# Kernel optimization log

Hardware: AMD Instinct MI355X
Metric: run time of the kernel (lower is better)

The kernel has to match this reference:

```python
import jax, jax.numpy as jnp
import numpy as np

N, E, F_IN, D, L = 100000, 1600000, 32, 128, 5
B, V, T, EMB = 3000, 64, 128, 64
H = L * D  # 640 LSTM hidden
BN_EPS = 1e-5


def setup_inputs():
    key = jax.random.key(0)
    ks = jax.random.split(key, 20)
    rn = lambda k, s, sc=0.05: jax.random.normal(k, s, jnp.float32) * sc
    inp = {
        'x': jax.random.normal(ks[0], (N, F_IN), jnp.float32),
        'edge_index': jax.random.randint(ks[1], (2, E), 0, N, jnp.int32),
        'batch': jnp.sort(jax.random.randint(ks[2], (N,), 0, B, jnp.int32)),
        'smi': jax.random.randint(ks[3], (B, T), 0, V, jnp.int32),
        'gin0_w1': rn(ks[4], (F_IN, D)), 'gin0_b1': jnp.zeros((D,), jnp.float32),
        'gin0_w2': rn(ks[5], (D, D)),    'gin0_b2': jnp.zeros((D,), jnp.float32),
        'ginr_w1': rn(ks[6], (L - 1, D, D)), 'ginr_b1': jnp.zeros((L - 1, D), jnp.float32),
        'ginr_w2': rn(ks[7], (L - 1, D, D)), 'ginr_b2': jnp.zeros((L - 1, D), jnp.float32),
        'bn_gamma': jnp.ones((L, D), jnp.float32), 'bn_beta': jnp.zeros((L, D), jnp.float32),
        'emb': rn(ks[8], (V, EMB), 0.1).at[0].set(0.0),  # padding_idx=0
        'w_ih': rn(ks[9], (4 * H, EMB), 0.04), 'w_hh': rn(ks[10], (4 * H, H), 0.04),
        'b_ih': jnp.zeros((4 * H,), jnp.float32), 'b_hh': jnp.zeros((4 * H,), jnp.float32),
        'g_w1': rn(ks[11], (L * D, 4 * D)), 'g_b1': jnp.zeros((4 * D,), jnp.float32),
        'g_bn_gamma': jnp.ones((4 * D,), jnp.float32), 'g_bn_beta': jnp.zeros((4 * D,), jnp.float32),
        'g_w2': rn(ks[12], (4 * D, 6 * D)),
    }
    return inp


def _bn(h, gamma, beta):
    # BatchNorm1d in training mode: biased batch statistics
    mu = h.mean(0)
    var = h.var(0)
    return (h - mu) * jax.lax.rsqrt(var + BN_EPS) * gamma + beta


def _gin_layer(h, src, dst, w1, b1, w2, b2, gamma, beta):
    # GINConv (eps=0): MLP(x + sum_{j->i} x_j), then ReLU, then BN
    agg = jax.ops.segment_sum(h[src], dst, num_segments=N)  # [N, d]
    z = h + agg
    z = jnp.maximum(z @ w1 + b1, 0.0) @ w2 + b2
    z = jnp.maximum(z, 0.0)
    return _bn(z, gamma, beta)


def _lstm_last(e, w_ih, w_hh, b_ih, b_hh):
    # e: [B, T, EMB] -> last hidden state [B, H]
    def step(carry, xt):
        h, c = carry
        gates = xt @ w_ih.T + b_ih + h @ w_hh.T + b_hh  # [B, 4H]
        i, f, g, o = jnp.split(gates, 4, axis=1)  # torch gate order i,f,g,o
        c = jax.nn.sigmoid(f) * c + jax.nn.sigmoid(i) * jnp.tanh(g)
        h = jax.nn.sigmoid(o) * jnp.tanh(c)
        return (h, c), None
    h0 = jnp.zeros((e.shape[0], H), e.dtype)
    (h, _), _ = jax.lax.scan(step, (h0, h0), e.transpose(1, 0, 2))
    return h


def reference(x, edge_index, batch, smi, gin0_w1, gin0_b1, gin0_w2, gin0_b2,
              ginr_w1, ginr_b1, ginr_w2, ginr_b2, bn_gamma, bn_beta, emb,
              w_ih, w_hh, b_ih, b_hh, g_w1, g_b1, g_bn_gamma, g_bn_beta, g_w2):
    src, dst = edge_index[0], edge_index[1]
    # --- GIN encoder with layer-wise global_add_pool ---
    h = _gin_layer(x, src, dst, gin0_w1, gin0_b1, gin0_w2, gin0_b2, bn_gamma[0], bn_beta[0])
    pools = [jax.ops.segment_sum(h, batch, num_segments=B)]
    for i in range(L - 1):
        h = _gin_layer(h, src, dst, ginr_w1[i], ginr_b1[i], ginr_w2[i], ginr_b2[i],
                       bn_gamma[i + 1], bn_beta[i + 1])
        pools.append(jax.ops.segment_sum(h, batch, num_segments=B))
    enc1 = jnp.concatenate(pools, axis=1)  # [B, L*D]
    # --- SMILES encoder: Embedding + LSTM, take output at last timestep ---
    enc2 = _lstm_last(emb[smi], w_ih, w_hh, b_ih, b_hh)  # [B, H] == [B, L*D]
    # --- shared projection head g, L2-normalized (F.normalize, eps=1e-12) ---
    def g_head(z):
        z1 = jnp.maximum(_bn(z @ g_w1 + g_b1, g_bn_gamma, g_bn_beta), 0.0)
        out = z1 @ g_w2
        nrm = jnp.maximum(jnp.linalg.norm(out, axis=1, keepdims=True), 1e-12)
        return out / nrm
    return (g_head(enc1), g_head(enc2))
```

## Files before the change

kernel.cpp:

```cpp
#include <hip/hip_runtime.h>

typedef __bf16 bf16x8 __attribute__((ext_vector_type(8)));
typedef float f32x4 __attribute__((ext_vector_type(4)));
typedef unsigned short ushort8 __attribute__((ext_vector_type(8)));

#define DEV static __device__ __forceinline__

DEV unsigned short f2bf(float f){
  unsigned int u = __builtin_bit_cast(unsigned int, f);
  u += 0x7fffu + ((u >> 16) & 1u);
  return (unsigned short)(u >> 16);
}
DEV float bf2f(unsigned short u){
  return __builtin_bit_cast(float, ((unsigned int)u) << 16);
}
DEV float sigf(float x){ return 1.0f/(1.0f + __expf(-x)); }

static constexpr int NN   = 100000;
static constexpr int NPAD = 100096;
static constexpr int NE   = 1600000;
static constexpr int NB   = 3000;
static constexpr int BPAD = 3072;
static constexpr int TT   = 128;
static constexpr int HID  = 640;
static constexpr int SCAN_B = 1024;
static constexpr int NBLK = (NN + SCAN_B - 1)/SCAN_B;

__global__ void cvt_k(const float* __restrict__ s, unsigned short* __restrict__ d, int n){
  int i = blockIdx.x*256 + threadIdx.x; if (i < n) d[i] = f2bf(s[i]);
}
__global__ void transpose_cvt_split_k(const float* __restrict__ s, unsigned short* __restrict__ dh,
                                      unsigned short* __restrict__ dl, int R, int C){
  int i = blockIdx.x*256 + threadIdx.x; if (i >= R*C) return;
  int r = i / C, c = i - r*C;
  float v = s[i];
  unsigned short hi = f2bf(v);
  dh[c*R + r] = hi;
  dl[c*R + r] = f2bf(v - bf2f(hi));
}
__global__ void wc_build_k(const float* __restrict__ whh, const float* __restrict__ wih,
                           unsigned short* __restrict__ wc){
  int i = blockIdx.x*256 + threadIdx.x; if (i >= 2560*704) return;
  int n = i / 704, k = i - n*704;
  float v = (k < 640) ? whh[n*640 + k] : wih[n*64 + (k - 640)];
  wc[i] = f2bf(v);
}
__global__ void add_k(const float* __restrict__ a, const float* __restrict__ b, float* __restrict__ o, int n){
  int i = blockIdx.x*256 + threadIdx.x; if (i < n) o[i] = a[i] + b[i];
}

__global__ __launch_bounds__(256) void deg_hist_k(const int* __restrict__ dsts, int* __restrict__ deg){
  int e = blockIdx.x*256 + threadIdx.x; if (e < NE) atomicAdd(&deg[dsts[e]], 1);
}
__global__ __launch_bounds__(256) void scan_bsum_k(const int* __restrict__ deg, int* __restrict__ bsum){
  __shared__ int red[4];
  int b = blockIdx.x, tid = threadIdx.x;
  int base = b*SCAN_B + tid*4;
  int s = 0;
  #pragma unroll
  for (int q = 0; q < 4; ++q){ int idx = base + q; s += (idx < NN) ? deg[idx] : 0; }
  #pragma unroll
  for (int m = 1; m < 64; m <<= 1) s += __shfl_xor(s, m);
  if ((tid & 63) == 0) red[tid >> 6] = s;
  __syncthreads();
  if (tid == 0) bsum[b] = red[0] + red[1] + red[2] + red[3];
}
__global__ void scan_off_k(int* __restrict__ bsum){
  if (threadIdx.x == 0){
    int run = 0;
    for (int i = 0; i < NBLK; ++i){ int t = bsum[i]; bsum[i] = run; run += t; }
  }
}
__global__ __launch_bounds__(256) void scan_write_k(const int* __restrict__ deg, const int* __restrict__ bsum,
                                                    int* __restrict__ rowptr, int* __restrict__ cursor){
  __shared__ int tsum[256];
  int b = blockIdx.x, tid = threadIdx.x;
  int base = b*SCAN_B + tid*4;
  int v[4]; int s = 0;
  #pragma unroll
  for (int q = 0; q < 4; ++q){ int idx = base + q; v[q] = (idx < NN) ? deg[idx] : 0; s += v[q]; }
  tsum[tid] = s;
  __syncthreads();
  for (int offt = 1; offt < 256; offt <<= 1){
    int y = (tid >= offt) ? tsum[tid - offt] : 0;
    __syncthreads();
    tsum[tid] += y;
    __syncthreads();
  }
  int run = bsum[b] + tsum[tid] - s;
  #pragma unroll
  for (int q = 0; q < 4; ++q){
    int idx = base + q;
    if (idx < NN){ rowptr[idx] = run; cursor[idx] = run; }
    run += v[q];
  }
  if (b == 0 && tid == 0) rowptr[NN] = NE;
}
__global__ __launch_bounds__(256) void csr_fill_k(const int* __restrict__ srcs, const int* __restrict__ dsts,
                                                  int* __restrict__ cursor, int* __restrict__ eidx){
  int e = blockIdx.x*256 + threadIdx.x; if (e >= NE) return;
  int d = dsts[e];
  int pos = atomicAdd(&cursor[d], 1);
  eidx[pos] = srcs[e];
}

__global__ __launch_bounds__(256) void gbound_k(const int* __restrict__ batch, int* __restrict__ gstart){
  int i = blockIdx.x*256 + threadIdx.x;
  if (i >= NN) return;
  int bi = batch[i];
  int bp = (i == 0) ? -1 : batch[i-1];
  for (int g = bp + 1; g <= bi; ++g) gstart[g] = i;
  if (i == NN-1){
    for (int g = bi + 1; g <= NB; ++g) gstart[g] = NN;
  }
}

__global__ __launch_bounds__(256) void agg128_k(const int* __restrict__ rowptr, const int* __restrict__ eidx,
    const float* __restrict__ H, float* __restrict__ Z){
  int wid = (blockIdx.x*256 + threadIdx.x) >> 6;
  if (wid >= NN) return;
  int lane = threadIdx.x & 63;
  const float2* Hp = (const float2*)H;
  int n0 = rowptr[wid], n1 = rowptr[wid+1];
  float2 acc = Hp[(size_t)wid*64 + lane];
  int i = n0;
  for (; i + 1 < n1; i += 2){
    int s0 = eidx[i], s1 = eidx[i+1];
    float2 v0 = Hp[(size_t)s0*64 + lane];
    float2 v1 = Hp[(size_t)s1*64 + lane];
    acc.x += v0.x + v1.x; acc.y += v0.y + v1.y;
  }
  if (i < n1){
    float2 v = Hp[(size_t)eidx[i]*64 + lane];
    acc.x += v.x; acc.y += v.y;
  }
  ((float2*)Z)[(size_t)wid*64 + lane] = acc;
}
__global__ __launch_bounds__(256) void agg32_k(const int* __restrict__ rowptr, const int* __restrict__ eidx,
    const float* __restrict__ X, float* __restrict__ Z){
  int r = (blockIdx.x*256 + threadIdx.x) >> 5;
  if (r >= NN) return;
  int l = threadIdx.x & 31;
  int n0 = rowptr[r], n1 = rowptr[r+1];
  float acc = X[(size_t)r*32 + l];
  int i = n0;
  for (; i + 1 < n1; i += 2){
    int s0 = eidx[i], s1 = eidx[i+1];
    acc += X[(size_t)s0*32 + l] + X[(size_t)s1*32 + l];
  }
  if (i < n1) acc += X[(size_t)eidx[i]*32 + l];
  Z[(size_t)r*32 + l] = acc;
}

template<int KIN>
__global__ __launch_bounds__(256) void gin_mlp_k(const float* __restrict__ Z,
    const unsigned short* __restrict__ W1h, const unsigned short* __restrict__ W1l,
    const unsigned short* __restrict__ W2h, const unsigned short* __restrict__ W2l,
    const float* __restrict__ b1, const float* __restrict__ b2,
    float* __restrict__ Y, float* __restrict__ stats)
{
  constexpr int SA = KIN + 8;
  __shared__ __align__(16) unsigned short Ah[128*136];
  __shared__ __align__(16) unsigned short Al[128*136];
  const int tid = threadIdx.x, lane = tid & 63, w = tid >> 6;
  const int row0 = blockIdx.x * 128;
  const int wr = (w >> 1)*64, wc0 = (w & 1)*64;
  const int l15 = lane & 15, lg = lane >> 4;

  constexpr int CH = KIN/8;
  #pragma unroll
  for (int i = 0; i < (128*CH)/256; ++i){
    int chunk = tid + 256*i;
    int row = chunk / CH, kc = (chunk - row*CH)*8;
    const float* sp = Z + (size_t)(row0 + row)*KIN + kc;
    float4 a0 = *(const float4*)sp;
    float4 a1 = *(const float4*)(sp + 4);
    float vv[8] = {a0.x,a0.y,a0.z,a0.w,a1.x,a1.y,a1.z,a1.w};
    ushort8 vh, vl;
    #pragma unroll
    for (int q=0;q<8;++q){ unsigned short h = f2bf(vv[q]); vh[q]=h; vl[q]=f2bf(vv[q]-bf2f(h)); }
    *(ushort8*)&Ah[row*SA + kc] = vh;
    *(ushort8*)&Al[row*SA + kc] = vl;
  }
  __syncthreads();

  f32x4 acc[4][4];
  #pragma unroll
  for (int i=0;i<4;++i)
    #pragma unroll
    for (int j=0;j<4;++j) acc[i][j] = (f32x4)(0.0f);

  #pragma unroll
  for (int k0 = 0; k0 < KIN; k0 += 32){
    bf16x8 ah[4], al[4], bh[4], bl[4];
    #pragma unroll
    for (int fa=0; fa<4; ++fa){
      ah[fa] = *(const bf16x8*)&Ah[(wr + fa*16 + l15)*SA + k0 + 8*lg];
      al[fa] = *(const bf16x8*)&Al[(wr + fa*16 + l15)*SA + k0 + 8*lg];
    }
    #pragma unroll
    for (int fb=0; fb<4; ++fb){
      bh[fb] = *(const bf16x8*)&W1h[(wc0 + fb*16 + l15)*KIN + k0 + 8*lg];
      bl[fb] = *(const bf16x8*)&W1l[(wc0 + fb*16 + l15)*KIN + k0 + 8*lg];
    }
    #pragma unroll
    for (int fa=0; fa<4; ++fa)
      #pragma unroll
      for (int fb=0; fb<4; ++fb){
        acc[fa][fb] = __builtin_amdgcn_mfma_f32_16x16x32_bf16(ah[fa], bh[fb], acc[fa][fb], 0, 0, 0);
        acc[fa][fb] = __builtin_amdgcn_mfma_f32_16x16x32_bf16(al[fa], bh[fb], acc[fa][fb], 0, 0, 0);
        acc[fa][fb] = __builtin_amdgcn_mfma_f32_16x16x32_bf16(ah[fa], bl[fb], acc[fa][fb], 0, 0, 0);
      }
  }
  __syncthreads();

  {
    float b1v[4];
    #pragma unroll
    for (int fb=0; fb<4; ++fb) b1v[fb] = b1[wc0 + fb*16 + l15];
    #pragma unroll
    for (int fa=0; fa<4; ++fa)
      #pragma unroll
      for (int fb=0; fb<4; ++fb)
        #pragma unroll
        for (int r=0; r<4; ++r){
          float v = fmaxf(acc[fa][fb][r] + b1v[fb], 0.0f);
          unsigned short h = f2bf(v);
          int idx = (wr + fa*16 + lg*4 + r)*136 + (wc0 + fb*16 + l15);
          Ah[idx] = h;
          Al[idx] = f2bf(v - bf2f(h));
        }
  }
  __syncthreads();

  f32x4 acc2[4][4];
  #pragma unroll
  for (int i=0;i<4;++i)
    #pragma unroll
    for (int j=0;j<4;++j) acc2[i][j] = (f32x4)(0.0f);

  #pragma unroll
  for (int k0 = 0; k0 < 128; k0 += 32){
    bf16x8 ah[4], al[4], bh[4], bl[4];
    #pragma unroll
    for (int fa=0; fa<4; ++fa){
      ah[fa] = *(const bf16x8*)&Ah[(wr + fa*16 + l15)*136 + k0 + 8*lg];
      al[fa] = *(const bf16x8*)&Al[(wr + fa*16 + l15)*136 + k0 + 8*lg];
    }
    #pragma unroll
    for (int fb=0; fb<4; ++fb){
      bh[fb] = *(const bf16x8*)&W2h[(wc0 + fb*16 + l15)*128 + k0 + 8*lg];
      bl[fb] = *(const bf16x8*)&W2l[(wc0 + fb*16 + l15)*128 + k0 + 8*lg];
    }
    #pragma unroll
    for (int fa=0; fa<4; ++fa)
      #pragma unroll
      for (int fb=0; fb<4; ++fb){
        acc2[fa][fb] = __builtin_amdgcn_mfma_f32_16x16x32_bf16(ah[fa], bh[fb], acc2[fa][fb], 0, 0, 0);
        acc2[fa][fb] = __builtin_amdgcn_mfma_f32_16x16x32_bf16(al[fa], bh[fb], acc2[fa][fb], 0, 0, 0);
        acc2[fa][fb] = __builtin_amdgcn_mfma_f32_16x16x32_bf16(ah[fa], bl[fb], acc2[fa][fb], 0, 0, 0);
      }
  }

  float b2v[4]; int cc[4];
  #pragma unroll
  for (int fb=0; fb<4; ++fb){ cc[fb] = wc0 + fb*16 + l15; b2v[fb] = b2[cc[fb]]; }
  float ps[4] = {0,0,0,0}, pq[4] = {0,0,0,0};
  #pragma unroll
  for (int fa=0; fa<4; ++fa)
    #pragma unroll
    for (int fb=0; fb<4; ++fb)
      #pragma unroll
      for (int r=0; r<4; ++r){
        int row = row0 + wr + fa*16 + lg*4 + r;
        float v = fmaxf(acc2[fa][fb][r] + b2v[fb], 0.0f);
        if (row < NN){
          Y[(size_t)row*128 + cc[fb]] = v;
          ps[fb] += v; pq[fb] += v*v;
        }
      }
  #pragma unroll
  for (int fb=0; fb<4; ++fb){
    float s = ps[fb]; s += __shfl_xor(s, 16); s += __shfl_xor(s, 32);
    float q = pq[fb]; q += __shfl_xor(q, 16); q += __shfl_xor(q, 32);
    if (lane < 16){ atomicAdd(&stats[cc[fb]], s); atomicAdd(&stats[128 + cc[fb]], q); }
  }
}

__global__ void bn_finalize_k(const float* __restrict__ stats, const float* __restrict__ gamma,
                              const float* __restrict__ beta, float* __restrict__ sshift, int C, float invN){
  int c = blockIdx.x*blockDim.x + threadIdx.x; if (c >= C) return;
  float mean = stats[c]*invN;
  float var  = fmaxf(stats[C+c]*invN - mean*mean, 0.0f);
  float inv  = rsqrtf(var + 1e-5f);
  float sc   = gamma[c]*inv;
  sshift[c] = sc; sshift[C+c] = beta[c] - mean*sc;
}

__global__ __launch_bounds__(256) void bn_apply_k(const float* __restrict__ Y,
    const float* __restrict__ sshift, float* __restrict__ Hb)
{
  int gid = blockIdx.x*256 + threadIdx.x;
  int r = gid >> 5;
  if (r >= NN) return;
  int c0 = (gid & 31) << 2;
  float4 y = *(const float4*)&Y[(size_t)r*128 + c0];
  float4 h;
  h.x = y.x*sshift[c0+0] + sshift[128+c0+0];
  h.y = y.y*sshift[c0+1] + sshift[128+c0+1];
  h.z = y.z*sshift[c0+2] + sshift[128+c0+2];
  h.w = y.w*sshift[c0+3] + sshift[128+c0+3];
  *(float4*)&Hb[(size_t)r*128 + c0] = h;
}

__global__ __launch_bounds__(256) void pool_seg_k(const float* __restrict__ Hb,
    const int* __restrict__ gstart, float* __restrict__ pool, int layer)
{
  int g = blockIdx.x*4 + (threadIdx.x >> 6);
  if (g >= NB) return;
  int lane = threadIdx.x & 63;
  int n0 = gstart[g], n1 = gstart[g+1];
  const float2* Hp = (const float2*)Hb;
  float2 acc = make_float2(0.f, 0.f);
  for (int r = n0; r < n1; ++r){
    float2 v = Hp[(size_t)r*64 + lane];
    acc.x += v.x; acc.y += v.y;
  }
  ((float2*)pool)[(size_t)g*320 + layer*64 + lane] = acc;
}

__global__ __launch_bounds__(256) void embed_k(const int* __restrict__ smi,
    const unsigned short* __restrict__ emb_bf, unsigned short* __restrict__ e_bf){
  int gid = blockIdx.x*256 + threadIdx.x;
  int b = gid >> 11;
  if (b >= BPAD) return;
  int t = (gid >> 4) & 127;
  int k4 = (gid & 15) << 2;
  uint2 v = make_uint2(0u, 0u);
  if (b < NB){
    int tok = smi[b*TT + t];
    v = *(const uint2*)&emb_bf[tok*64 + k4];
  }
  *(uint2*)&e_bf[(size_t)(b*TT + t)*64 + k4] = v;
}

__global__ __launch_bounds__(256) void lstm_step_k(const unsigned short* __restrict__ hprev,
    unsigned short* __restrict__ hnext, float* __restrict__ cbuf,
    const unsigned short* __restrict__ ebf, const unsigned short* __restrict__ Wc,
    const float* __restrict__ biasc, int t, float* __restrict__ hfin)
{
  __shared__ __align__(16) unsigned short As[128*40];
  __shared__ __align__(16) unsigned short Bs[128*40];
  const int tid = threadIdx.x, lane = tid & 63, w = tid >> 6;
  const int row0 = blockIdx.x * 128;
  const int j0 = blockIdx.y * 32;
  const int l15 = lane & 15, lg = lane >> 4;

  f32x4 acc[2][8];
  #pragma unroll
  for (int i=0;i<2;++i)
    #pragma unroll
    for (int j=0;j<8;++j) acc[i][j] = (f32x4)(0.0f);

  for (int kk = 0; kk < 22; ++kk){
    const int k0 = kk*32;
    #pragma unroll
    for (int i = 0; i < 2; ++i){
      int chunk = tid + 256*i;
      int row = chunk >> 2, kc = (chunk & 3) << 3;
      ushort8 v;
      if (k0 < 640) v = *(const ushort8*)&hprev[(size_t)(row0+row)*HID + k0 + kc];
      else          v = *(const ushort8*)&ebf[(size_t)((row0+row)*TT + t)*64 + (k0-640) + kc];
      *(ushort8*)&As[row*40 + kc] = v;
      int c = row;
      int ng = (c >> 5)*640 + j0 + (c & 31);
      *(ushort8*)&Bs[c*40 + kc] = *(const ushort8*)&Wc[(size_t)ng*704 + k0 + kc];
    }
    __syncthreads();
    bf16x8 a[2], b[8];
    #pragma unroll
    for (int fa=0; fa<2; ++fa) a[fa] = *(const bf16x8*)&As[(w*32 + fa*16 + l15)*40 + 8*lg];
    #pragma unroll
    for (int fb=0; fb<8; ++fb) b[fb] = *(const bf16x8*)&Bs[(fb*16 + l15)*40 + 8*lg];
    #pragma unroll
    for (int fa=0; fa<2; ++fa)
      #pragma unroll
      for (int fb=0; fb<8; ++fb)
        acc[fa][fb] = __builtin_amdgcn_mfma_f32_16x16x32_bf16(a[fa], b[fb], acc[fa][fb], 0, 0, 0);
    __syncthreads();
  }

  #pragma unroll
  for (int fa=0; fa<2; ++fa){
    #pragma unroll
    for (int par=0; par<2; ++par){
      int jj = j0 + par*16 + l15;
      float bi = biasc[jj], bf_ = biasc[640+jj], bg = biasc[1280+jj], bo = biasc[1920+jj];
      #pragma unroll
      for (int r=0; r<4; ++r){
        int br = row0 + w*32 + fa*16 + lg*4 + r;
        float iv = acc[fa][0+par][r] + bi;
        float fv = acc[fa][2+par][r] + bf_;
        float gv = acc[fa][4+par][r] + bg;
        float ov = acc[fa][6+par][r] + bo;
        size_t idx = (size_t)br*HID + jj;
        float co = cbuf[idx];
        float cn = sigf(fv)*co + sigf(iv)*tanhf(gv);
        cbuf[idx] = cn;
        float hv = sigf(ov)*tanhf(cn);
        hnext[idx] = f2bf(hv);
        if (hfin) hfin[idx] = hv;
      }
    }
  }
}

template<int DO_STATS>
__global__ __launch_bounds__(256) void gemm_split_k(const float* __restrict__ A,
    const unsigned short* __restrict__ Bh, const unsigned short* __restrict__ Bl,
    const float* __restrict__ bias, float* __restrict__ outp, float* __restrict__ stats,
    int Mvalid, int Nc, int K)
{
  __shared__ __align__(16) unsigned short Ah[128*40];
  __shared__ __align__(16) unsigned short Al[128*40];
  const int tid = threadIdx.x, lane = tid & 63, w = tid >> 6;
  const int row0 = blockIdx.x * 128, col0 = blockIdx.y * 128;
  const int wr = (w >> 1)*64, wc0 = (w & 1)*64;
  const int l15 = lane & 15, lg = lane >> 4;

  f32x4 acc[4][4];
  #pragma unroll
  for (int i=0;i<4;++i)
    #pragma unroll
    for (int j=0;j<4;++j) acc[i][j] = (f32x4)(0.0f);

  for (int k0 = 0; k0 < K; k0 += 32){
    #pragma unroll
    for (int i=0;i<2;++i){
      int chunk = tid + 256*i;
      int row = chunk >> 2, kc = (chunk & 3) << 3;
      const float* sp = A + (size_t)(row0+row)*K + k0 + kc;
      float4 a0 = *(const float4*)sp;
      float4 a1 = *(const float4*)(sp + 4);
      float vv[8] = {a0.x,a0.y,a0.z,a0.w,a1.x,a1.y,a1.z,a1.w};
      ushort8 vh, vl;
      #pragma unroll
      for (int q=0;q<8;++q){ unsigned short h = f2bf(vv[q]); vh[q]=h; vl[q]=f2bf(vv[q]-bf2f(h)); }
      *(ushort8*)&Ah[row*40 + kc] = vh;
      *(ushort8*)&Al[row*40 + kc] = vl;
    }
    __syncthreads();
    bf16x8 ah[4], al[4], bh[4], bl[4];
    #pragma unroll
    for (int fa=0; fa<4; ++fa){
      ah[fa] = *(const bf16x8*)&Ah[(wr + fa*16 + l15)*40 + 8*lg];
      al[fa] = *(const bf16x8*)&Al[(wr + fa*16 + l15)*40 + 8*lg];
    }
    #pragma unroll
    for (int fb=0; fb<4; ++fb){
      bh[fb] = *(const bf16x8*)&Bh[(size_t)(col0 + wc0 + fb*16 + l15)*K + k0 + 8*lg];
      bl[fb] = *(const bf16x8*)&Bl[(size_t)(col0 + wc0 + fb*16 + l15)*K + k0 + 8*lg];
    }
    #pragma unroll
    for (int fa=0; fa<4; ++fa)
      #pragma unroll
      for (int fb=0; fb<4; ++fb){
        acc[fa][fb] = __builtin_amdgcn_mfma_f32_16x16x32_bf16(ah[fa], bh[fb], acc[fa][fb], 0, 0, 0);
        acc[fa][fb] = __builtin_amdgcn_mfma_f32_16x16x32_bf16(al[fa], bh[fb], acc[fa][fb], 0, 0, 0);
        acc[fa][fb] = __builtin_amdgcn_mfma_f32_16x16x32_bf16(ah[fa], bl[fb], acc[fa][fb], 0, 0, 0);
      }
    __syncthreads();
  }

  float bv[4]; int cc[4];
  #pragma unroll
  for (int fb=0; fb<4; ++fb){ cc[fb] = col0 + wc0 + fb*16 + l15; bv[fb] = bias ? bias[cc[fb]] : 0.0f; }
  float ps[4] = {0,0,0,0}, pq[4] = {0,0,0,0};
  #pragma unroll
  for (int fa=0; fa<4; ++fa)
    #pragma unroll
    for (int fb=0; fb<4; ++fb)
      #pragma unroll
      for (int r=0; r<4; ++r){
        int row = row0 + wr + fa*16 + lg*4 + r;
        float v = acc[fa][fb][r] + bv[fb];
        if (row < Mvalid){
          outp[(size_t)row*Nc + cc[fb]] = v;
          if (DO_STATS){ ps[fb] += v; pq[fb] += v*v; }
        }
      }
  if (DO_STATS){
    #pragma unroll
    for (int fb=0; fb<4; ++fb){
      float s = ps[fb]; s += __shfl_xor(s, 16); s += __shfl_xor(s, 32);
      float q = pq[fb]; q += __shfl_xor(q, 16); q += __shfl_xor(q, 32);
      if (lane < 16){ atomicAdd(&stats[cc[fb]], s); atomicAdd(&stats[Nc + cc[fb]], q); }
    }
  }
}

__global__ __launch_bounds__(256) void bn_apply_head_k(const float* __restrict__ Zpre,
    const float* __restrict__ sshift, float* __restrict__ z1f){
  int gid = blockIdx.x*256 + threadIdx.x;
  int r = gid >> 7;
  if (r >= BPAD) return;
  int c0 = (gid & 127) << 2;
  float4 o = make_float4(0.f,0.f,0.f,0.f);
  if (r < NB){
    float4 v = *(const float4*)&Zpre[(size_t)r*512 + c0];
    o.x = fmaxf(v.x*sshift[c0+0] + sshift[512+c0+0], 0.0f);
    o.y = fmaxf(v.y*sshift[c0+1] + sshift[512+c0+1], 0.0f);
    o.z = fmaxf(v.z*sshift[c0+2] + sshift[512+c0+2], 0.0f);
    o.w = fmaxf(v.w*sshift[c0+3] + sshift[512+c0+3], 0.0f);
  }
  *(float4*)&z1f[(size_t)r*512 + c0] = o;
}

__global__ __launch_bounds__(256) void rownorm_k(const float* __restrict__ in, float* __restrict__ outp){
  int r = blockIdx.x;
  const float* p = in + (size_t)r*768;
  float ss = 0.0f;
  #pragma unroll
  for (int i = 0; i < 3; ++i){ float v = p[threadIdx.x + 256*i]; ss += v*v; }
  #pragma unroll
  for (int m = 1; m < 64; m <<= 1) ss += __shfl_xor(ss, m);
  __shared__ float red[4];
  if ((threadIdx.x & 63) == 0) red[threadIdx.x >> 6] = ss;
  __syncthreads();
  float tot = red[0] + red[1] + red[2] + red[3];
  float inv = 1.0f / fmaxf(sqrtf(tot), 1e-12f);
  float* q = outp + (size_t)r*768;
  #pragma unroll
  for (int i = 0; i < 3; ++i) q[threadIdx.x + 256*i] = p[threadIdx.x + 256*i]*inv;
}

static inline int cdiv(long a, long b){ return (int)((a + b - 1)/b); }

extern "C" void kernel_launch(void* const* d_in, const int* in_sizes, int n_in,
                              void* d_out, int out_size, void* d_ws, size_t ws_size,
                              hipStream_t stream)
{
  const float* x        = (const float*)d_in[0];
  const int*   edges    = (const int*)d_in[1];
  const int*   batch    = (const int*)d_in[2];
  const int*   smi      = (const int*)d_in[3];
  const float* gin0_w1  = (const float*)d_in[4];
  const float* gin0_b1  = (const float*)d_in[5];
  const float* gin0_w2  = (const float*)d_in[6];
  const float* gin0_b2  = (const float*)d_in[7];
  const float* ginr_w1  = (const float*)d_in[8];
  const float* ginr_b1  = (const float*)d_in[9];
  const float* ginr_w2  = (const float*)d_in[10];
  const float* ginr_b2  = (const float*)d_in[11];
  const float* bn_gamma = (const float*)d_in[12];
  const float* bn_beta  = (const float*)d_in[13];
  const float* emb      = (const float*)d_in[14];
  const float* w_ih     = (const float*)d_in[15];
  const float* w_hh     = (const float*)d_in[16];
  const float* b_ih     = (const float*)d_in[17];
  const float* b_hh     = (const float*)d_in[18];
  const float* g_w1     = (const float*)d_in[19];
  const float* g_b1     = (const float*)d_in[20];
  const float* g_bng    = (const float*)d_in[21];
  const float* g_bnb    = (const float*)d_in[22];
  const float* g_w2     = (const float*)d_in[23];
  float* outp = (float*)d_out;
  const int* srcs = edges;
  const int* dsts = edges + NE;

  char* base = (char*)d_ws;
  size_t off = 0;
  auto carve = [&](size_t bytes)->char*{ char* p = base + off; off += (bytes + 255) & ~(size_t)255; return p; };
  float* z_gin = (float*)carve((size_t)NPAD*128*4);
  float* y_gin = (float*)carve((size_t)NPAD*128*4);
  float* h_gin = (float*)carve((size_t)NPAD*128*4);
  float* pool  = (float*)carve((size_t)BPAD*HID*4);
  unsigned short* Wc     = (unsigned short*)carve((size_t)2560*704*2);
  float*          biasc  = (float*)carve(2560*4);
  unsigned short* emb_bf = (unsigned short*)carve(4096*2);
  unsigned short* w1t0h  = (unsigned short*)carve(128*32*2);
  unsigned short* w1t0l  = (unsigned short*)carve(128*32*2);
  unsigned short* w2t0h  = (unsigned short*)carve(128*128*2);
  unsigned short* w2t0l  = (unsigned short*)carve(128*128*2);
  unsigned short* w1trh  = (unsigned short*)carve(4*16384*2);
  unsigned short* w1trl  = (unsigned short*)carve(4*16384*2);
  unsigned short* w2trh  = (unsigned short*)carve(4*16384*2);
  unsigned short* w2trl  = (unsigned short*)carve(4*16384*2);
  unsigned short* gw1th  = (unsigned short*)carve(512*640*2);
  unsigned short* gw1tl  = (unsigned short*)carve(512*640*2);
  unsigned short* gw2th  = (unsigned short*)carve(768*512*2);
  unsigned short* gw2tl  = (unsigned short*)carve(768*512*2);
  float* stats  = (float*)carve(1024*4);
  float* sshift = (float*)carve(1024*4);
  int* deg    = (int*)carve((size_t)NN*4);
  int* cursor = (int*)carve((size_t)NN*4);
  int* rowptr = (int*)carve((size_t)(NN+1)*4);
  int* bsum   = (int*)carve(512);
  int* eidx   = (int*)carve((size_t)NE*4);
  int* gstart = (int*)carve((size_t)(NB+1)*4);

  unsigned short* e_bf   = (unsigned short*)y_gin;
  unsigned short* h_a    = (unsigned short*)h_gin;
  unsigned short* h_b    = h_a + (size_t)BPAD*HID;
  float*          c_buf  = (float*)(h_b + (size_t)BPAD*HID);
  float*          hfin   = c_buf + (size_t)BPAD*HID;
  float*          z1pre  = (float*)z_gin;
  float*          z1f    = z1pre + (size_t)BPAD*512;
  float*          outtmp = z1f + (size_t)BPAD*512;

  wc_build_k<<<cdiv((long)2560*704,256),256,0,stream>>>(w_hh, w_ih, Wc);
  add_k<<<cdiv(2560,256),256,0,stream>>>(b_ih, b_hh, biasc, 2560);
  cvt_k<<<cdiv(4096,256),256,0,stream>>>(emb, emb_bf, 4096);
  transpose_cvt_split_k<<<cdiv(32*128,256),256,0,stream>>>(gin0_w1, w1t0h, w1t0l, 32, 128);
  transpose_cvt_split_k<<<cdiv(16384,256),256,0,stream>>>(gin0_w2, w2t0h, w2t0l, 128, 128);
  for (int i = 0; i < 4; ++i){
    transpose_cvt_split_k<<<cdiv(16384,256),256,0,stream>>>(ginr_w1 + (size_t)i*16384, w1trh + (size_t)i*16384, w1trl + (size_t)i*16384, 128, 128);
    transpose_cvt_split_k<<<cdiv(16384,256),256,0,stream>>>(ginr_w2 + (size_t)i*16384, w2trh + (size_t)i*16384, w2trl + (size_t)i*16384, 128, 128);
  }
  transpose_cvt_split_k<<<cdiv(640*512,256),256,0,stream>>>(g_w1, gw1th, gw1tl, 640, 512);
  transpose_cvt_split_k<<<cdiv(512*768,256),256,0,stream>>>(g_w2, gw2th, gw2tl, 512, 768);

  hipMemsetAsync(deg, 0, (size_t)NN*4, stream);
  deg_hist_k<<<cdiv(NE,256),256,0,stream>>>(dsts, deg);
  scan_bsum_k<<<NBLK,256,0,stream>>>(deg, bsum);
  scan_off_k<<<1,64,0,stream>>>(bsum);
  scan_write_k<<<NBLK,256,0,stream>>>(deg, bsum, rowptr, cursor);
  csr_fill_k<<<cdiv(NE,256),256,0,stream>>>(srcs, dsts, cursor, eidx);
  gbound_k<<<cdiv(NN,256),256,0,stream>>>(batch, gstart);

  for (int l = 0; l < 5; ++l){
    hipMemsetAsync(stats, 0, 1024*4, stream);
    if (l == 0)
      agg32_k<<<cdiv((long)NN*32,256),256,0,stream>>>(rowptr, eidx, x, z_gin);
    else
      agg128_k<<<cdiv((long)NN*64,256),256,0,stream>>>(rowptr, eidx, h_gin, z_gin);
    if (l == 0)
      gin_mlp_k<32><<<NPAD/128,256,0,stream>>>(z_gin, w1t0h, w1t0l, w2t0h, w2t0l, gin0_b1, gin0_b2, y_gin, stats);
    else
      gin_mlp_k<128><<<NPAD/128,256,0,stream>>>(z_gin, w1trh + (size_t)(l-1)*16384, w1trl + (size_t)(l-1)*16384,
                                                w2trh + (size_t)(l-1)*16384, w2trl + (size_t)(l-1)*16384,
                                                ginr_b1 + (l-1)*128, ginr_b2 + (l-1)*128, y_gin, stats);
    bn_finalize_k<<<1,128,0,stream>>>(stats, bn_gamma + l*128, bn_beta + l*128, sshift, 128, 1.0f/NN);
    bn_apply_k<<<cdiv((long)NN*32,256),256,0,stream>>>(y_gin, sshift, h_gin);
    pool_seg_k<<<cdiv(NB,4),256,0,stream>>>(h_gin, gstart, pool, l);
  }

  embed_k<<<cdiv((long)BPAD*TT*16,256),256,0,stream>>>(smi, emb_bf, e_bf);
  hipMemsetAsync(h_a, 0, (size_t)BPAD*HID*2, stream);
  hipMemsetAsync(c_buf, 0, (size_t)BPAD*HID*4, stream);
  for (int t = 0; t < TT; ++t){
    const unsigned short* hin = (t & 1) ? h_b : h_a;
    unsigned short* hout      = (t & 1) ? h_a : h_b;
    lstm_step_k<<<dim3(BPAD/128, 20),256,0,stream>>>(hin, hout, c_buf, e_bf, Wc, biasc, t,
                                                     (t == TT-1) ? hfin : nullptr);
  }

  const float* headAf[2] = { pool, hfin };
  for (int hd = 0; hd < 2; ++hd){
    hipMemsetAsync(stats, 0, 1024*4, stream);
    gemm_split_k<1><<<dim3(BPAD/128, 4),256,0,stream>>>(headAf[hd], gw1th, gw1tl, g_b1, z1pre, stats, NB, 512, 640);
    bn_finalize_k<<<2,256,0,stream>>>(stats, g_bng, g_bnb, sshift, 512, 1.0f/NB);
    bn_apply_head_k<<<cdiv((long)BPAD*128,256),256,0,stream>>>(z1pre, sshift, z1f);
    gemm_split_k<0><<<dim3(BPAD/128, 6),256,0,stream>>>(z1f, gw2th, gw2tl, nullptr, outtmp, nullptr, NB, 768, 512);
    rownorm_k<<<NB,256,0,stream>>>(outtmp, outp + (size_t)hd*NB*768);
  }
}
```

Baseline: 4.965 ms.

## Double-buffer LSTM step GEMM and pre-permute gate weights into contiguous tiles

The LSTM step kernel now uses double-buffered LDS tiles, issuing global loads for the next K-slice into registers while MFMAs run on the current slice. It also moves from a 2x8 to a 2x2 wave layout with 4x4 fragments per wave. To support this, the combined W_hh/W_ih weight matrix is permuted once so each block's 128 gate rows are contiguous. The embedding buffer is reordered to time-major so each step reads a contiguous slab. The cost is twice the LDS use, which may lower occupancy, and more index math in the one-time weight build.

```diff
diff --git a/kernel.cpp b/kernel.cpp
--- a/kernel.cpp
+++ b/kernel.cpp
@@ -38,12 +38,15 @@
   dh[c*R + r] = hi;
   dl[c*R + r] = f2bf(v - bf2f(hi));
 }
-__global__ void wc_build_k(const float* __restrict__ whh, const float* __restrict__ wih,
-                           unsigned short* __restrict__ wc){
+__global__ void wc2_build_k(const float* __restrict__ whh, const float* __restrict__ wih,
+                            unsigned short* __restrict__ wc2){
   int i = blockIdx.x*256 + threadIdx.x; if (i >= 2560*704) return;
-  int n = i / 704, k = i - n*704;
+  int n2 = i / 704, k = i - n2*704;
+  int jt = n2 >> 7, rem = n2 & 127;
+  int hc = rem >> 6, gate = (rem >> 4) & 3, j15 = rem & 15;
+  int n = gate*640 + jt*32 + hc*16 + j15;
   float v = (k < 640) ? whh[n*640 + k] : wih[n*64 + (k - 640)];
-  wc[i] = f2bf(v);
+  wc2[i] = f2bf(v);
 }
 __global__ void add_k(const float* __restrict__ a, const float* __restrict__ b, float* __restrict__ o, int n){
   int i = blockIdx.x*256 + threadIdx.x; if (i < n) o[i] = a[i] + b[i];
@@ -330,87 +333,106 @@
 }
 
 __global__ __launch_bounds__(256) void embed_k(const int* __restrict__ smi,
-    const unsigned short* __restrict__ emb_bf, unsigned short* __restrict__ e_bf){
+    const unsigned short* __restrict__ emb_bf, unsigned short* __restrict__ e2){
   int gid = blockIdx.x*256 + threadIdx.x;
-  int b = gid >> 11;
-  if (b >= BPAD) return;
-  int t = (gid >> 4) & 127;
+  int tb = gid >> 4;
+  if (tb >= TT*BPAD) return;
+  int t = tb / BPAD, b = tb - t*BPAD;
   int k4 = (gid & 15) << 2;
   uint2 v = make_uint2(0u, 0u);
   if (b < NB){
     int tok = smi[b*TT + t];
     v = *(const uint2*)&emb_bf[tok*64 + k4];
   }
-  *(uint2*)&e_bf[(size_t)(b*TT + t)*64 + k4] = v;
+  *(uint2*)&e2[(size_t)tb*64 + k4] = v;
 }
 
 __global__ __launch_bounds__(256) void lstm_step_k(const unsigned short* __restrict__ hprev,
     unsigned short* __restrict__ hnext, float* __restrict__ cbuf,
-    const unsigned short* __restrict__ ebf, const unsigned short* __restrict__ Wc,
+    const unsigned short* __restrict__ e2, const unsigned short* __restrict__ Wc2,
     const float* __restrict__ biasc, int t, float* __restrict__ hfin)
 {
-  __shared__ __align__(16) unsigned short As[128*40];
-  __shared__ __align__(16) unsigned short Bs[128*40];
+  __shared__ __align__(16) unsigned short As[2][128*40];
+  __shared__ __align__(16) unsigned short Bs[2][128*40];
   const int tid = threadIdx.x, lane = tid & 63, w = tid >> 6;
   const int row0 = blockIdx.x * 128;
-  const int j0 = blockIdx.y * 32;
+  const int jt = blockIdx.y;
   const int l15 = lane & 15, lg = lane >> 4;
-
-  f32x4 acc[2][8];
-  #pragma unroll
-  for (int i=0;i<2;++i)
-    #pragma unroll
-    for (int j=0;j<8;++j) acc[i][j] = (f32x4)(0.0f);
-
+  const int wr = (w >> 1)*64, wc0 = (w & 1)*64;
+
+  const int srow = tid >> 2, skc = (tid & 3) << 3;
+  const unsigned short* A0 = hprev + (size_t)(row0 + srow)*HID;
+  const unsigned short* A1 = hprev + (size_t)(row0 + srow + 64)*HID;
+  const unsigned short* E0 = e2 + ((size_t)t*BPAD + row0 + srow)*64;
+  const unsigned short* E1 = e2 + ((size_t)t*BPAD + row0 + srow + 64)*64;
+  const unsigned short* B0 = Wc2 + (size_t)(jt*128 + srow)*704;
+  const unsigned short* B1 = Wc2 + (size_t)(jt*128 + srow + 64)*704;
+
+  *(ushort8*)&As[0][srow*40 + skc]      = *(const ushort8*)&A0[skc];
+  *(ushort8*)&As[0][(srow+64)*40 + skc] = *(const ushort8*)&A1[skc];
+  *(ushort8*)&Bs[0][srow*40 + skc]      = *(const ushort8*)&B0[skc];
+  *(ushort8*)&Bs[0][(srow+64)*40 + skc] = *(const ushort8*)&B1[skc];
+  __syncthreads();
+
+  f32x4 acc[4][4];
+  #pragma unroll
+  for (int i=0;i<4;++i)
+    #pragma unroll
+    for (int j=0;j<4;++j) acc[i][j] = (f32x4)(0.0f);
+
+  int p = 0;
   for (int kk = 0; kk < 22; ++kk){
-    const int k0 = kk*32;
-    #pragma unroll
-    for (int i = 0; i < 2; ++i){
-      int chunk = tid + 256*i;
-      int row = chunk >> 2, kc = (chunk & 3) << 3;
-      ushort8 v;
-      if (k0 < 640) v = *(const ushort8*)&hprev[(size_t)(row0+row)*HID + k0 + kc];
-      else          v = *(const ushort8*)&ebf[(size_t)((row0+row)*TT + t)*64 + (k0-640) + kc];
-      *(ushort8*)&As[row*40 + kc] = v;
-      int c = row;
-      int ng = (c >> 5)*640 + j0 + (c & 31);
-      *(ushort8*)&Bs[c*40 + kc] = *(const ushort8*)&Wc[(size_t)ng*704 + k0 + kc];
+    ushort8 va0, va1, vb0, vb1;
+    const int k1 = (kk+1)*32;
+    if (kk < 21){
+      if (k1 < 640){
+        va0 = *(const ushort8*)&A0[k1 + skc];
+        va1 = *(const ushort8*)&A1[k1 + skc];
+      } else {
+        va0 = *(const ushort8*)&E0[k1 - 640 + skc];
+        va1 = *(const ushort8*)&E1[k1 - 640 + skc];
+      }
+      vb0 = *(const ushort8*)&B0[k1 + skc];
+      vb1 = *(const ushort8*)&B1[k1 + skc];
+    }
+    bf16x8 a[4], b[4];
+    #pragma unroll
+    for (int fa=0; fa<4; ++fa) a[fa] = *(const bf16x8*)&As[p][(wr + fa*16 + l15)*40 + 8*lg];
+    #pragma unroll
+    for (int fb=0; fb<4; ++fb) b[fb] = *(const bf16x8*)&Bs[p][(wc0 + fb*16 + l15)*40 + 8*lg];
+    #pragma unroll
+    for (int fa=0; fa<4; ++fa)
+      #pragma unroll
+      for (int fb=0; fb<4; ++fb)
+        acc[fa][fb] = __builtin_amdgcn_mfma_f32_16x16x32_bf16(a[fa], b[fb], acc[fa][fb], 0, 0, 0);
+    if (kk < 21){
+      *(ushort8*)&As[p^1][srow*40 + skc]      = va0;
+      *(ushort8*)&As[p^1][(srow+64)*40 + skc] = va1;
+      *(ushort8*)&Bs[p^1][srow*40 + skc]      = vb0;
+      *(ushort8*)&Bs[p^1][(srow+64)*40 + skc] = vb1;
     }
     __syncthreads();
-    bf16x8 a[2], b[8];
-    #pragma unroll
-    for (int fa=0; fa<2; ++fa) a[fa] = *(const bf16x8*)&As[(w*32 + fa*16 + l15)*40 + 8*lg];
-    #pragma unroll
-    for (int fb=0; fb<8; ++fb) b[fb] = *(const bf16x8*)&Bs[(fb*16 + l15)*40 + 8*lg];
-    #pragma unroll
-    for (int fa=0; fa<2; ++fa)
-      #pragma unroll
-      for (int fb=0; fb<8; ++fb)
-        acc[fa][fb] = __builtin_amdgcn_mfma_f32_16x16x32_bf16(a[fa], b[fb], acc[fa][fb], 0, 0, 0);
-    __syncthreads();
-  }
-
-  #pragma unroll
-  for (int fa=0; fa<2; ++fa){
-    #pragma unroll
-    for (int par=0; par<2; ++par){
-      int jj = j0 + par*16 + l15;
-      float bi = biasc[jj], bf_ = biasc[640+jj], bg = biasc[1280+jj], bo = biasc[1920+jj];
-      #pragma unroll
-      for (int r=0; r<4; ++r){
-        int br = row0 + w*32 + fa*16 + lg*4 + r;
-        float iv = acc[fa][0+par][r] + bi;
-        float fv = acc[fa][2+par][r] + bf_;
-        float gv = acc[fa][4+par][r] + bg;
-        float ov = acc[fa][6+par][r] + bo;
-        size_t idx = (size_t)br*HID + jj;
-        float co = cbuf[idx];
-        float cn = sigf(fv)*co + sigf(iv)*tanhf(gv);
-        cbuf[idx] = cn;
-        float hv = sigf(ov)*tanhf(cn);
-        hnext[idx] = f2bf(hv);
-        if (hfin) hfin[idx] = hv;
-      }
+    p ^= 1;
+  }
+
+  const int j = jt*32 + (w & 1)*16 + l15;
+  float bi = biasc[j], bf_ = biasc[640+j], bg = biasc[1280+j], bo = biasc[1920+j];
+  #pragma unroll
+  for (int fa=0; fa<4; ++fa){
+    #pragma unroll
+    for (int r=0; r<4; ++r){
+      int br = row0 + wr + fa*16 + lg*4 + r;
+      float iv = acc[fa][0][r] + bi;
+      float fv = acc[fa][1][r] + bf_;
+      float gv = acc[fa][2][r] + bg;
+      float ov = acc[fa][3][r] + bo;
+      size_t idx = (size_t)br*HID + j;
+      float co = cbuf[idx];
+      float cn = sigf(fv)*co + sigf(iv)*tanhf(gv);
+      cbuf[idx] = cn;
+      float hv = sigf(ov)*tanhf(cn);
+      hnext[idx] = f2bf(hv);
+      if (hfin) hfin[idx] = hv;
     }
   }
 }
@@ -575,7 +597,7 @@
   float* y_gin = (float*)carve((size_t)NPAD*128*4);
   float* h_gin = (float*)carve((size_t)NPAD*128*4);
   float* pool  = (float*)carve((size_t)BPAD*HID*4);
-  unsigned short* Wc     = (unsigned short*)carve((size_t)2560*704*2);
+  unsigned short* Wc2    = (unsigned short*)carve((size_t)2560*704*2);
   float*          biasc  = (float*)carve(2560*4);
   unsigned short* emb_bf = (unsigned short*)carve(4096*2);
   unsigned short* w1t0h  = (unsigned short*)carve(128*32*2);
@@ -599,7 +621,7 @@
   int* eidx   = (int*)carve((size_t)NE*4);
   int* gstart = (int*)carve((size_t)(NB+1)*4);
 
-  unsigned short* e_bf   = (unsigned short*)y_gin;
+  unsigned short* e2     = (unsigned short*)y_gin;
   unsigned short* h_a    = (unsigned short*)h_gin;
   unsigned short* h_b    = h_a + (size_t)BPAD*HID;
   float*          c_buf  = (float*)(h_b + (size_t)BPAD*HID);
@@ -608,7 +630,7 @@
   float*          z1f    = z1pre + (size_t)BPAD*512;
   float*          outtmp = z1f + (size_t)BPAD*512;
 
-  wc_build_k<<<cdiv((long)2560*704,256),256,0,stream>>>(w_hh, w_ih, Wc);
+  wc2_build_k<<<cdiv((long)2560*704,256),256,0,stream>>>(w_hh, w_ih, Wc2);
   add_k<<<cdiv(2560,256),256,0,stream>>>(b_ih, b_hh, biasc, 2560);
   cvt_k<<<cdiv(4096,256),256,0,stream>>>(emb, emb_bf, 4096);
   transpose_cvt_split_k<<<cdiv(32*128,256),256,0,stream>>>(gin0_w1, w1t0h, w1t0l, 32, 128);
@@ -645,13 +667,13 @@
     pool_seg_k<<<cdiv(NB,4),256,0,stream>>>(h_gin, gstart, pool, l);
   }
 
-  embed_k<<<cdiv((long)BPAD*TT*16,256),256,0,stream>>>(smi, emb_bf, e_bf);
+  embed_k<<<cdiv((long)TT*BPAD*16,256),256,0,stream>>>(smi, emb_bf, e2);
   hipMemsetAsync(h_a, 0, (size_t)BPAD*HID*2, stream);
   hipMemsetAsync(c_buf, 0, (size_t)BPAD*HID*4, stream);
   for (int t = 0; t < TT; ++t){
     const unsigned short* hin = (t & 1) ? h_b : h_a;
     unsigned short* hout      = (t & 1) ? h_a : h_b;
-    lstm_step_k<<<dim3(BPAD/128, 20),256,0,stream>>>(hin, hout, c_buf, e_bf, Wc, biasc, t,
+    lstm_step_k<<<dim3(BPAD/128, 20),256,0,stream>>>(hin, hout, c_buf, e2, Wc2, biasc, t,
                                                      (t == TT-1) ? hfin : nullptr);
   }
 
```

Result: faster. 4.749 ms (-4.3%).
